# Optimization experiments

Hardware: AMD Instinct MI355X
Metric: run time of the kernel (lower is better)

## Reference

```python
import jax, jax.numpy as jnp
import numpy as np

NUM_EXPERTS = 64
TOPK = 8
EPS = 1.1920929e-07  # torch.finfo(float32).eps


def setup_inputs() -> dict:
    key = jax.random.key(0)
    k1, k2 = jax.random.split(key)
    hidden_states = jax.random.normal(k1, (1, 4096, 4096), dtype=jnp.float32)
    wg_weight = jax.random.normal(k2, (NUM_EXPERTS, 4096), dtype=jnp.float32) * 0.02
    return {"hidden_states": hidden_states, "wg_weight": wg_weight}


def _routing(logits, capacity):
    # logits: [T, E]; capacity: static python int
    gates = jax.nn.softmax(logits, axis=1)                       # [T, E]
    _, idx = jax.lax.top_k(gates, TOPK)                          # [T, k]
    emask = jax.nn.one_hot(idx, NUM_EXPERTS, dtype=jnp.float32)  # [T, k, E]
    # sum of selected gate probs per token, clamped at fp32 eps
    gates_s = jnp.clip(jnp.einsum('tke,te->t', emask, gates), EPS)[:, None]
    router_probs = gates / gates_s                               # [T, E]
    # priority: cumulative position of each token within each expert,
    # scanned over (topk-major, token-minor) flattened order
    idx_flat = idx.T.reshape(-1)                                 # [k*T]
    mflat = jax.nn.one_hot(idx_flat, NUM_EXPERTS, dtype=jnp.int32)
    tp = jnp.cumsum(mflat, axis=0) * mflat - 1                   # [k*T, E]
    tp = tp.reshape(TOPK, -1, NUM_EXPERTS).transpose(1, 0, 2).max(axis=1)  # [T, E]
    valid = (tp >= 0) & (tp < capacity)                          # [T, E]
    tp = jnp.where(valid, tp, 0)
    dispatch_mask = jax.nn.one_hot(tp, capacity, dtype=jnp.bool_) & valid[:, :, None]  # [T, E, C]
    combine_weights = router_probs[:, :, None] * dispatch_mask   # [T, E, C]
    return combine_weights, dispatch_mask


def reference(hidden_states, wg_weight):
    b, s, h = hidden_states.shape
    x = hidden_states.reshape(-1, h).astype(jnp.float32)         # [T, H]
    logits = x @ wg_weight.T                                     # [T, E]
    # expert_capacity = max tokens assigned to any expert (data-dependent,
    # computed eagerly as in the torch .item() call)
    _, idx = jax.lax.top_k(jax.nn.softmax(logits, axis=1), TOPK)
    counts = jnp.bincount(idx.reshape(-1), length=NUM_EXPERTS)
    capacity = int(counts.max())
    return _routing(logits, capacity)
```

## Files before the change

kernel.cpp:

```cpp
#include <hip/hip_runtime.h>
#include <hip/hip_bf16.h>


#define TOK 4096
#define HID 4096
#define NE  64
#define NK  8
#define NSPLIT 8

typedef __attribute__((ext_vector_type(8))) short short8;
typedef __attribute__((ext_vector_type(4))) float f32x4;

__device__ __forceinline__ short f2bf(float f) {
  __hip_bfloat16 h = __float2bfloat16(f);
  return *reinterpret_cast<short*>(&h);
}
__device__ __forceinline__ float bf2f(short s) {
  unsigned u = ((unsigned)(unsigned short)s) << 16;
  return __uint_as_float(u);
}
__device__ __forceinline__ void cvt3(float f, short& s0, short& s1, short& s2) {
  s0 = f2bf(f);
  float r1 = f - bf2f(s0);
  s1 = f2bf(r1);
  float r2 = r1 - bf2f(s1);
  s2 = f2bf(r2);
}

__global__ __launch_bounds__(256) void mega(
    const float* __restrict__ x, const float* __restrict__ wg,
    double* __restrict__ partial, int kchunk, int ngemm, int nfill,
    float* __restrict__ out, int out_n) {
  const int bx  = blockIdx.x;
  const int tid = threadIdx.x;

  if (bx >= ngemm) {
    const int    fid    = bx - ngemm;
    const size_t n4     = ((size_t)(unsigned)out_n) >> 2;
    const size_t stride = (size_t)nfill * 256;
    f32x4* o4 = (f32x4*)out;
    const f32x4 z4 = (f32x4){0.f, 0.f, 0.f, 0.f};
    size_t i = (size_t)fid * 256 + tid;
    for (; i + 3 * stride < n4; i += 4 * stride) {
      o4[i]              = z4;
      o4[i + stride]     = z4;
      o4[i + 2 * stride] = z4;
      o4[i + 3 * stride] = z4;
    }
    for (; i < n4; i += stride) o4[i] = z4;
    if (fid == 0 && tid == 0)
      for (size_t i2 = n4 << 2; i2 < (size_t)(unsigned)out_n; ++i2) out[i2] = 0.f;
    return;
  }

  __shared__ __align__(16) short XA[3][64][72];
  __shared__ __align__(16) short WB[3][64][72];
  const int tileid = bx & 63;
  const int slab   = bx >> 6;
  const int t0   = tileid * 64;
  const int k0   = slab * kchunk;
  const int lane = tid & 63;
  const int w    = tid >> 6;
  const int m    = lane & 15;
  const int q    = lane >> 4;
  const int lrow = tid >> 2;
  const int lq   = tid & 3;

  f32x4 acc[4];
#pragma unroll
  for (int nt = 0; nt < 4; ++nt) acc[nt] = (f32x4){0.f, 0.f, 0.f, 0.f};

  for (int s = 0; s < kchunk; s += 64) {
    const int kk = k0 + s;
#pragma unroll
    for (int c = 0; c < 4; ++c) {
      const int col = lq * 16 + c * 4;
      float4 xv = *(const float4*)&x [(size_t)(t0 + lrow) * HID + kk + col];
      float4 wv = *(const float4*)&wg[(size_t)lrow * HID + kk + col];
      short4 p0, p1, p2;
      cvt3(xv.x, p0.x, p1.x, p2.x);  cvt3(xv.y, p0.y, p1.y, p2.y);
      cvt3(xv.z, p0.z, p1.z, p2.z);  cvt3(xv.w, p0.w, p1.w, p2.w);
      *(short4*)&XA[0][lrow][col] = p0;
      *(short4*)&XA[1][lrow][col] = p1;
      *(short4*)&XA[2][lrow][col] = p2;
      cvt3(wv.x, p0.x, p1.x, p2.x);  cvt3(wv.y, p0.y, p1.y, p2.y);
      cvt3(wv.z, p0.z, p1.z, p2.z);  cvt3(wv.w, p0.w, p1.w, p2.w);
      *(short4*)&WB[0][lrow][col] = p0;
      *(short4*)&WB[1][lrow][col] = p1;
      *(short4*)&WB[2][lrow][col] = p2;
    }
    __syncthreads();
#pragma unroll
    for (int kc = 0; kc < 64; kc += 32) {
      short8 a0 = *(const short8*)&XA[0][w * 16 + m][kc + q * 8];
      short8 a1 = *(const short8*)&XA[1][w * 16 + m][kc + q * 8];
      short8 a2 = *(const short8*)&XA[2][w * 16 + m][kc + q * 8];
#pragma unroll
      for (int nt = 0; nt < 4; ++nt) {
        short8 b0 = *(const short8*)&WB[0][nt * 16 + m][kc + q * 8];
        short8 b1 = *(const short8*)&WB[1][nt * 16 + m][kc + q * 8];
        short8 b2 = *(const short8*)&WB[2][nt * 16 + m][kc + q * 8];
        acc[nt] = __builtin_amdgcn_mfma_f32_16x16x32_bf16(a0, b0, acc[nt], 0, 0, 0);
        acc[nt] = __builtin_amdgcn_mfma_f32_16x16x32_bf16(a0, b1, acc[nt], 0, 0, 0);
        acc[nt] = __builtin_amdgcn_mfma_f32_16x16x32_bf16(a1, b0, acc[nt], 0, 0, 0);
        acc[nt] = __builtin_amdgcn_mfma_f32_16x16x32_bf16(a0, b2, acc[nt], 0, 0, 0);
        acc[nt] = __builtin_amdgcn_mfma_f32_16x16x32_bf16(a1, b1, acc[nt], 0, 0, 0);
        acc[nt] = __builtin_amdgcn_mfma_f32_16x16x32_bf16(a2, b0, acc[nt], 0, 0, 0);
      }
    }
    __syncthreads();
  }

  double* base = partial + (size_t)slab * TOK * NE;
#pragma unroll
  for (int nt = 0; nt < 4; ++nt)
#pragma unroll
    for (int v = 0; v < 4; ++v)
      base[(size_t)(t0 + w * 16 + q * 4 + v) * NE + nt * 16 + m] =
          (double)acc[nt][v];
}

__global__ __launch_bounds__(256) void topk_kernel(
    const double* __restrict__ partial, int nsplit,
    int* __restrict__ idx8, float* __restrict__ w8) {
  const int gid  = blockIdx.x * blockDim.x + threadIdx.x;
  const int t    = gid >> 6;
  const int lane = gid & 63;

  double v = 0.0;
  for (int p = 0; p < nsplit; ++p)
    v += partial[(size_t)p * TOK * NE + (size_t)t * NE + lane];

  double m = v;
#pragma unroll
  for (int off = 32; off; off >>= 1) {
    double o = __shfl_xor(m, off);
    m = o > m ? o : m;
  }
  double g = exp(v - m);
  double s = g;
#pragma unroll
  for (int off = 32; off; off >>= 1) s += __shfl_xor(s, off);
  double gate = g / s;

  float key = (float)gate;
  double ssel = 0.0;
  int my_k = -1;
#pragma unroll
  for (int k = 0; k < NK; ++k) {
    float bv = key;
    int   bi = lane;
#pragma unroll
    for (int off = 32; off; off >>= 1) {
      float ov = __shfl_xor(bv, off);
      int   oi = __shfl_xor(bi, off);
      if (ov > bv || (ov == bv && oi < bi)) { bv = ov; bi = oi; }
    }
    ssel += __shfl(gate, bi);
    if (lane == bi) { my_k = k; key = -1.0f; }
  }
  double gs = ssel;
  const double eps = (double)1.1920929e-07f;
  if (gs < eps) gs = eps;

  if (my_k >= 0) {
    idx8[t * 8 + my_k] = lane;
    w8 [t * 8 + my_k] = (float)(gate / gs);
  }
}

__global__ __launch_bounds__(1024) void scatter2(
    const int* __restrict__ idx8, const float* __restrict__ w8,
    float* __restrict__ out, int C) {
  const int e   = blockIdx.x;
  const int tid = threadIdx.x;
  __shared__ int sa[1024];
  __shared__ int sb[1024];

  const int base = tid * 32;
  const int k    = base >> 12;
  const int tbase = base & (TOK - 1);
  unsigned mask = 0u;
  int cnt = 0;
#pragma unroll 8
  for (int s = 0; s < 32; ++s) {
    if (idx8[(tbase + s) * 8 + k] == e) { mask |= (1u << s); ++cnt; }
  }

  sa[tid] = cnt;
  __syncthreads();
  int* src = sa; int* dst = sb;
  for (int off = 1; off < 1024; off <<= 1) {
    int v = src[tid];
    if (tid >= off) v += src[tid - off];
    dst[tid] = v;
    __syncthreads();
    int* tmp = src; src = dst; dst = tmp;
  }
  int c = src[tid] - cnt;

  for (unsigned mm = mask; mm; mm &= (mm - 1)) {
    const int s = __builtin_ctz(mm);
    const int t = tbase + s;
    if (c < C) {
      const float wv = w8[t * 8 + k];
      const size_t off2 = ((size_t)t * NE + e) * (size_t)C + (size_t)c;
      out[off2] = wv;
      out[(size_t)TOK * NE * C + off2] = 1.0f;
    }
    ++c;
  }
}

extern "C" void kernel_launch(void* const* d_in, const int* in_sizes, int n_in,
                              void* d_out, int out_size, void* d_ws, size_t ws_size,
                              hipStream_t stream) {
  const float* x  = (const float*)d_in[0];
  const float* wg = (const float*)d_in[1];
  float* out = (float*)d_out;

  const int C = out_size / (2 * TOK * NE);

  char* ws = (char*)d_ws;
  double* partial = (double*)ws;
  const size_t psz = (size_t)NSPLIT * TOK * NE * sizeof(double);
  int*    idx8 = (int*)  (ws + psz);
  float*  w8   = (float*)(ws + psz + (size_t)NK * TOK * sizeof(int));

  const int kchunk = HID / NSPLIT;
  const int ngemm  = 64 * NSPLIT;
  const int nfill  = 2048;

  mega       <<<ngemm + nfill, 256, 0, stream>>>(x, wg, partial, kchunk,
                                                 ngemm, nfill, out, out_size);
  topk_kernel<<<TOK * 64 / 256, 256, 0, stream>>>(partial, NSPLIT, idx8, w8);
  scatter2   <<<NE, 1024, 0, stream>>>(idx8, w8, out, C);
}
```

Baseline: 1.268 ms.

## Fuse softmax/top-k into GEMM epilogue and drop split-K partials

Removes the split-K decomposition so each of 64 GEMM blocks accumulates over the full hidden dimension, promoting fp32 MFMA accumulators to double every 512 columns. Softmax and top-8 selection are then computed in the GEMM epilogue via 16-lane shuffles, eliminating the separate topk kernel and the double-precision partial buffer. This trades GEMM parallelism (64 blocks instead of 512) for less memory traffic and one fewer launch, relying on the concurrent zero-fill blocks to hide the longer GEMM.

```diff
diff --git a/kernel.cpp b/kernel.cpp
--- a/kernel.cpp
+++ b/kernel.cpp
@@ -6,7 +6,6 @@
 #define HID 4096
 #define NE  64
 #define NK  8
-#define NSPLIT 8
 
 typedef __attribute__((ext_vector_type(8))) short short8;
 typedef __attribute__((ext_vector_type(4))) float f32x4;
@@ -29,13 +28,13 @@
 
 __global__ __launch_bounds__(256) void mega(
     const float* __restrict__ x, const float* __restrict__ wg,
-    double* __restrict__ partial, int kchunk, int ngemm, int nfill,
+    int* __restrict__ idx8, float* __restrict__ w8, int nfill,
     float* __restrict__ out, int out_n) {
   const int bx  = blockIdx.x;
   const int tid = threadIdx.x;
 
-  if (bx >= ngemm) {
-    const int    fid    = bx - ngemm;
+  if (bx >= 64) {
+    const int    fid    = bx - 64;
     const size_t n4     = ((size_t)(unsigned)out_n) >> 2;
     const size_t stride = (size_t)nfill * 256;
     f32x4* o4 = (f32x4*)out;
@@ -55,10 +54,7 @@
 
   __shared__ __align__(16) short XA[3][64][72];
   __shared__ __align__(16) short WB[3][64][72];
-  const int tileid = bx & 63;
-  const int slab   = bx >> 6;
-  const int t0   = tileid * 64;
-  const int k0   = slab * kchunk;
+  const int t0   = bx * 64;
   const int lane = tid & 63;
   const int w    = tid >> 6;
   const int m    = lane & 15;
@@ -67,11 +63,16 @@
   const int lq   = tid & 3;
 
   f32x4 acc[4];
-#pragma unroll
-  for (int nt = 0; nt < 4; ++nt) acc[nt] = (f32x4){0.f, 0.f, 0.f, 0.f};
-
-  for (int s = 0; s < kchunk; s += 64) {
-    const int kk = k0 + s;
+  double dacc[4][4];
+#pragma unroll
+  for (int nt = 0; nt < 4; ++nt) {
+    acc[nt] = (f32x4){0.f, 0.f, 0.f, 0.f};
+#pragma unroll
+    for (int v = 0; v < 4; ++v) dacc[nt][v] = 0.0;
+  }
+
+  for (int s = 0; s < HID; s += 64) {
+    const int kk = s;
 #pragma unroll
     for (int c = 0; c < 4; ++c) {
       const int col = lq * 16 + c * 4;
@@ -109,63 +110,62 @@
       }
     }
     __syncthreads();
-  }
-
-  double* base = partial + (size_t)slab * TOK * NE;
-#pragma unroll
-  for (int nt = 0; nt < 4; ++nt)
-#pragma unroll
-    for (int v = 0; v < 4; ++v)
-      base[(size_t)(t0 + w * 16 + q * 4 + v) * NE + nt * 16 + m] =
-          (double)acc[nt][v];
-}
-
-__global__ __launch_bounds__(256) void topk_kernel(
-    const double* __restrict__ partial, int nsplit,
-    int* __restrict__ idx8, float* __restrict__ w8) {
-  const int gid  = blockIdx.x * blockDim.x + threadIdx.x;
-  const int t    = gid >> 6;
-  const int lane = gid & 63;
-
-  double v = 0.0;
-  for (int p = 0; p < nsplit; ++p)
-    v += partial[(size_t)p * TOK * NE + (size_t)t * NE + lane];
-
-  double m = v;
-#pragma unroll
-  for (int off = 32; off; off >>= 1) {
-    double o = __shfl_xor(m, off);
-    m = o > m ? o : m;
-  }
-  double g = exp(v - m);
-  double s = g;
-#pragma unroll
-  for (int off = 32; off; off >>= 1) s += __shfl_xor(s, off);
-  double gate = g / s;
-
-  float key = (float)gate;
-  double ssel = 0.0;
-  int my_k = -1;
-#pragma unroll
-  for (int k = 0; k < NK; ++k) {
-    float bv = key;
-    int   bi = lane;
-#pragma unroll
-    for (int off = 32; off; off >>= 1) {
-      float ov = __shfl_xor(bv, off);
-      int   oi = __shfl_xor(bi, off);
-      if (ov > bv || (ov == bv && oi < bi)) { bv = ov; bi = oi; }
-    }
-    ssel += __shfl(gate, bi);
-    if (lane == bi) { my_k = k; key = -1.0f; }
-  }
-  double gs = ssel;
-  const double eps = (double)1.1920929e-07f;
-  if (gs < eps) gs = eps;
-
-  if (my_k >= 0) {
-    idx8[t * 8 + my_k] = lane;
-    w8 [t * 8 + my_k] = (float)(gate / gs);
+    if (((s >> 6) & 7) == 7) {
+#pragma unroll
+      for (int nt = 0; nt < 4; ++nt) {
+#pragma unroll
+        for (int v = 0; v < 4; ++v) dacc[nt][v] += (double)acc[nt][v];
+        acc[nt] = (f32x4){0.f, 0.f, 0.f, 0.f};
+      }
+    }
+  }
+
+#pragma unroll
+  for (int v = 0; v < 4; ++v) {
+    const int t = t0 + w * 16 + q * 4 + v;
+    double M = dacc[0][v];
+#pragma unroll
+    for (int nt = 1; nt < 4; ++nt) M = dacc[nt][v] > M ? dacc[nt][v] : M;
+#pragma unroll
+    for (int off = 1; off < 16; off <<= 1) {
+      double o = __shfl_xor(M, off);
+      M = o > M ? o : M;
+    }
+    double g64[4], S = 0.0;
+#pragma unroll
+    for (int nt = 0; nt < 4; ++nt) { g64[nt] = exp(dacc[nt][v] - M); S += g64[nt]; }
+#pragma unroll
+    for (int off = 1; off < 16; off <<= 1) S += __shfl_xor(S, off);
+    double gate[4]; float key[4];
+#pragma unroll
+    for (int nt = 0; nt < 4; ++nt) { gate[nt] = g64[nt] / S; key[nt] = (float)gate[nt]; }
+
+    double ssel = 0.0, my_g = 0.0; int my_e = 0;
+#pragma unroll
+    for (int k = 0; k < NK; ++k) {
+      float bk = key[0]; int bnt = 0;
+#pragma unroll
+      for (int nt = 1; nt < 4; ++nt)
+        if (key[nt] > bk) { bk = key[nt]; bnt = nt; }
+      int    be = bnt * 16 + m;
+      double bg = gate[bnt];
+#pragma unroll
+      for (int off = 1; off < 16; off <<= 1) {
+        float  ok = __shfl_xor(bk, off);
+        int    oe = __shfl_xor(be, off);
+        double og = __shfl_xor(bg, off);
+        if (ok > bk || (ok == bk && oe < be)) { bk = ok; be = oe; bg = og; }
+      }
+      ssel += bg;
+      if (m == (be & 15)) key[be >> 4] = -1.0f;
+      if (m == k) { my_e = be; my_g = bg; }
+    }
+    const double eps = (double)1.1920929e-07f;
+    double gs = ssel < eps ? eps : ssel;
+    if (m < NK) {
+      idx8[t * 8 + m] = my_e;
+      w8 [t * 8 + m] = (float)(my_g / gs);
+    }
   }
 }
 
@@ -221,18 +221,11 @@
 
   const int C = out_size / (2 * TOK * NE);
 
-  char* ws = (char*)d_ws;
-  double* partial = (double*)ws;
-  const size_t psz = (size_t)NSPLIT * TOK * NE * sizeof(double);
-  int*    idx8 = (int*)  (ws + psz);
-  float*  w8   = (float*)(ws + psz + (size_t)NK * TOK * sizeof(int));
-
-  const int kchunk = HID / NSPLIT;
-  const int ngemm  = 64 * NSPLIT;
-  const int nfill  = 2048;
-
-  mega       <<<ngemm + nfill, 256, 0, stream>>>(x, wg, partial, kchunk,
-                                                 ngemm, nfill, out, out_size);
-  topk_kernel<<<TOK * 64 / 256, 256, 0, stream>>>(partial, NSPLIT, idx8, w8);
-  scatter2   <<<NE, 1024, 0, stream>>>(idx8, w8, out, C);
-}
+  int*    idx8 = (int*)  d_ws;
+  float*  w8   = (float*)((char*)d_ws + (size_t)NK * TOK * sizeof(int));
+
+  const int nfill = 2048;
+
+  mega    <<<64 + nfill, 256, 0, stream>>>(x, wg, idx8, w8, nfill, out, out_size);
+  scatter2<<<NE, 1024, 0, stream>>>(idx8, w8, out, C);
+}
```

Result: slower. 1.316 ms (+3.8%).
